# Optimization experiments

Hardware: AMD Instinct MI355X
Metric: run time of the kernel (lower is better)

The kernel has to match this reference:

```python
import jax, jax.numpy as jnp
import numpy as np


def _fps_indices(xyz, num_points):
    """Furthest point sampling. xyz: [B, N, 3] -> indices [B, num_points] (int32)."""
    B, N, _ = xyz.shape

    def step(carry, _):
        dist, farthest = carry                                   # dist: [B, N], farthest: [B]
        centroid = jnp.take_along_axis(xyz, farthest[:, None, None], axis=1)  # [B, 1, 3]
        d = jnp.sum((xyz - centroid) ** 2, axis=-1)              # [B, N]
        dist = jnp.minimum(dist, d)
        nxt = jnp.argmax(dist, axis=-1).astype(jnp.int32)        # [B]
        return (dist, nxt), farthest

    init = (jnp.full((B, N), jnp.inf, dtype=xyz.dtype),
            jnp.zeros((B,), dtype=jnp.int32))                    # convention: start at index 0
    _, idxs = jax.lax.scan(step, init, None, length=num_points)  # [num_points, B]
    return idxs.T                                                # [B, num_points]


def setup_inputs() -> dict:
    key = jax.random.key(0)
    B, C, N = 16, 3, 131072
    points = jax.random.normal(key, (B, C, N), dtype=jnp.float32)
    return {"points": points, "num_points": 2048}


def reference(points, num_points):
    # points: [B, 3, N] channels-first, as in the torch module
    xyz = jnp.transpose(points, (0, 2, 1))                       # [B, N, 3]
    idx = _fps_indices(xyz, num_points)                          # [B, num_points]
    # fps_gather_by_index: gather along the point dim of the channels-first tensor
    new_points = jnp.take_along_axis(points, idx[:, None, :], axis=2)  # [B, 3, num_points]
    return new_points
```

## Files before the change

### kernel.cpp

```cpp
#include <hip/hip_runtime.h>
#include <stdint.h>


#define NBATCH    16
#define NPTS      131072
#define SUBBLOCKS 16
#define NTHREADS  1024
#define CHUNK     8192
#define HALF      4096

typedef unsigned long long u64;

__device__ __forceinline__ u64 umax64(u64 a, u64 b) { return a > b ? a : b; }

__global__ __launch_bounds__(NTHREADS, 4)
void fps_kernel(const float* __restrict__ points,
                float* __restrict__ out,
                u64* __restrict__ slots, int M)
{
  __shared__ u64 wkeys[NTHREADS / 64];
  __shared__ u64 winner_s;

  const int bid   = blockIdx.x;
  const int xcd   = bid & 7;
  const int ord   = bid >> 3;
  const int batch = xcd * 2 + (ord >> 4);
  const int sub   = ord & 15;
  const int tid   = threadIdx.x;
  const int wave  = tid >> 6;
  const int lane  = tid & 63;

  const float* __restrict__ px = points + (size_t)batch * 3 * NPTS;
  const float* __restrict__ py = px + NPTS;
  const float* __restrict__ pz = px + 2 * NPTS;
  float* outb = out + (size_t)batch * 3 * M;
  u64* bslots = slots + (size_t)batch * 2 * SUBBLOCKS;

  const int cbase = sub * CHUNK;
  const int g0 = cbase + (tid << 2);
  const int g1 = g0 + HALF;

  float4 A0 = *(const float4*)(px + g0);
  float4 B0 = *(const float4*)(py + g0);
  float4 C0 = *(const float4*)(pz + g0);
  float4 A1 = *(const float4*)(px + g1);
  float4 B1 = *(const float4*)(py + g1);
  float4 C1 = *(const float4*)(pz + g1);
  float x0=A0.x, x1=A0.y, x2=A0.z, x3=A0.w, x4=A1.x, x5=A1.y, x6=A1.z, x7=A1.w;
  float y0=B0.x, y1=B0.y, y2=B0.z, y3=B0.w, y4=B1.x, y5=B1.y, y6=B1.z, y7=B1.w;
  float z0=C0.x, z1=C0.y, z2=C0.z, z3=C0.w, z4=C1.x, z5=C1.y, z6=C1.z, z7=C1.w;
  asm volatile("" :
    "+v"(x0),"+v"(x1),"+v"(x2),"+v"(x3),"+v"(x4),"+v"(x5),"+v"(x6),"+v"(x7),
    "+v"(y0),"+v"(y1),"+v"(y2),"+v"(y3),"+v"(y4),"+v"(y5),"+v"(y6),"+v"(y7),
    "+v"(z0),"+v"(z1),"+v"(z2),"+v"(z3),"+v"(z4),"+v"(z5),"+v"(z6),"+v"(z7));

  float d0, d1, d2, d3, d4, d5, d6, d7;
  d0 = d1 = d2 = d3 = d4 = d5 = d6 = d7 = __builtin_inff();

  if (sub == 0 && tid == 0) {
    outb[0]     = px[0];
    outb[M]     = py[0];
    outb[2 * M] = pz[0];
  }

  int sel = 0;
  for (int t = 1; t < M; ++t) {
    float cx = px[sel], cy = py[sel], cz = pz[sel];

    float best = -1.0f;
    int bidx = 0;
#define STEP(XX, YY, ZZ, DREG, IDX) { \
    float dx = __fsub_rn((XX), cx); \
    float dy = __fsub_rn((YY), cy); \
    float dz = __fsub_rn((ZZ), cz); \
    float dd = __builtin_fmaf(dz, dz, __builtin_fmaf(dy, dy, __fmul_rn(dx, dx))); \
    DREG = DREG < dd ? DREG : dd; \
    if (DREG > best) { best = DREG; bidx = (IDX); } }
    STEP(x0, y0, z0, d0, g0 + 0)
    STEP(x1, y1, z1, d1, g0 + 1)
    STEP(x2, y2, z2, d2, g0 + 2)
    STEP(x3, y3, z3, d3, g0 + 3)
    STEP(x4, y4, z4, d4, g1 + 0)
    STEP(x5, y5, z5, d5, g1 + 1)
    STEP(x6, y6, z6, d6, g1 + 2)
    STEP(x7, y7, z7, d7, g1 + 3)

    u64 key = ((u64)__float_as_uint(best) << 17) | (u64)((NPTS - 1) - bidx);

#pragma unroll
    for (int m = 32; m >= 1; m >>= 1) {
      u64 o = __shfl_xor(key, m, 64);
      key = umax64(key, o);
    }
    if (lane == 0) wkeys[wave] = key;
    __syncthreads();

    if (wave == 0) {
      u64 k = wkeys[lane & 15];
#pragma unroll
      for (int m = 8; m >= 1; m >>= 1) {
        u64 o = __shfl_xor(k, m, 64);
        k = umax64(k, o);
      }
      u64* par = bslots + (size_t)(t & 1) * SUBBLOCKS;
      if (lane == 0) {
        __hip_atomic_store(par + sub, ((u64)t << 49) | k,
                           __ATOMIC_RELAXED, __HIP_MEMORY_SCOPE_AGENT);
      }
      const u64* pp = par + (lane & 15);
      u64 v;
      for (;;) {
        v = __hip_atomic_load(pp, __ATOMIC_RELAXED, __HIP_MEMORY_SCOPE_AGENT);
        if (__ballot((unsigned)(v >> 49) == (unsigned)t) == ~0ull) break;
      }
#pragma unroll
      for (int m = 8; m >= 1; m >>= 1) {
        u64 o = __shfl_xor(v, m, 64);
        v = umax64(v, o);
      }
      if (lane == 0) winner_s = v;
    }
    __syncthreads();

    sel = (NPTS - 1) - (int)(winner_s & 0x1FFFF);

    if (sub == 0 && tid == 0) {
      outb[t]         = px[sel];
      outb[M + t]     = py[sel];
      outb[2 * M + t] = pz[sel];
    }
  }
}

extern "C" void kernel_launch(void* const* d_in, const int* in_sizes, int n_in,
                              void* d_out, int out_size, void* d_ws, size_t ws_size,
                              hipStream_t stream) {
  (void)in_sizes; (void)n_in; (void)ws_size;
  const float* points = (const float*)d_in[0];
  float* out = (float*)d_out;
  u64* slots = (u64*)d_ws;
  const int M = out_size / (NBATCH * 3);

  hipMemsetAsync(d_ws, 0, (size_t)NBATCH * 2 * SUBBLOCKS * sizeof(u64), stream);

  hipLaunchKernelGGL(fps_kernel, dim3(NBATCH * SUBBLOCKS), dim3(NTHREADS), 0,
                     stream, points, out, slots, M);
}
```

Measured before the change: 4.174 ms.

## Carry winner coordinates through cross-block slots and poll from all waves

Each block now publishes the winning point's x/y/z alongside its key in the global slot array, four u64 words per block. Every wave polls the slots and reduces them itself instead of wave 0 polling and then broadcasting through a second __syncthreads. This drops the per-iteration dependent global load of the centroid coordinates (px[sel]) and one block barrier from the critical serial path. The cost is wider slot writes, heavier polling traffic from 16 waves per block, and extra select logic to pick the winning coordinates from registers.

```diff
diff --git a/kernel.cpp b/kernel.cpp
--- a/kernel.cpp
+++ b/kernel.cpp
@@ -6,8 +6,10 @@
 #define NPTS      131072
 #define SUBBLOCKS 16
 #define NTHREADS  1024
+#define NWAVES    (NTHREADS / 64)
 #define CHUNK     8192
 #define HALF      4096
+#define SLOTW     4
 
 typedef unsigned long long u64;
 
@@ -18,8 +20,7 @@
                 float* __restrict__ out,
                 u64* __restrict__ slots, int M)
 {
-  __shared__ u64 wkeys[NTHREADS / 64];
-  __shared__ u64 winner_s;
+  __shared__ u64 W[NWAVES][SLOTW];
 
   const int bid   = blockIdx.x;
   const int xcd   = bid & 7;
@@ -29,12 +30,13 @@
   const int tid   = threadIdx.x;
   const int wave  = tid >> 6;
   const int lane  = tid & 63;
+  const int role  = lane & 3;
 
   const float* __restrict__ px = points + (size_t)batch * 3 * NPTS;
   const float* __restrict__ py = px + NPTS;
   const float* __restrict__ pz = px + 2 * NPTS;
   float* outb = out + (size_t)batch * 3 * M;
-  u64* bslots = slots + (size_t)batch * 2 * SUBBLOCKS;
+  u64* bslots = slots + (size_t)batch * 2 * SUBBLOCKS * SLOTW;
 
   const int cbase = sub * CHUNK;
   const int g0 = cbase + (tid << 2);
@@ -57,77 +59,97 @@
   float d0, d1, d2, d3, d4, d5, d6, d7;
   d0 = d1 = d2 = d3 = d4 = d5 = d6 = d7 = __builtin_inff();
 
+  float cx = px[0], cy = py[0], cz = pz[0];
   if (sub == 0 && tid == 0) {
-    outb[0]     = px[0];
-    outb[M]     = py[0];
-    outb[2 * M] = pz[0];
+    outb[0]     = cx;
+    outb[M]     = cy;
+    outb[2 * M] = cz;
   }
 
-  int sel = 0;
   for (int t = 1; t < M; ++t) {
-    float cx = px[sel], cy = py[sel], cz = pz[sel];
-
     float best = -1.0f;
-    int bidx = 0;
-#define STEP(XX, YY, ZZ, DREG, IDX) { \
+    int bidx = 0, bj = 0;
+#define STEP(XX, YY, ZZ, DREG, IDX, J) { \
     float dx = __fsub_rn((XX), cx); \
     float dy = __fsub_rn((YY), cy); \
     float dz = __fsub_rn((ZZ), cz); \
     float dd = __builtin_fmaf(dz, dz, __builtin_fmaf(dy, dy, __fmul_rn(dx, dx))); \
     DREG = DREG < dd ? DREG : dd; \
-    if (DREG > best) { best = DREG; bidx = (IDX); } }
-    STEP(x0, y0, z0, d0, g0 + 0)
-    STEP(x1, y1, z1, d1, g0 + 1)
-    STEP(x2, y2, z2, d2, g0 + 2)
-    STEP(x3, y3, z3, d3, g0 + 3)
-    STEP(x4, y4, z4, d4, g1 + 0)
-    STEP(x5, y5, z5, d5, g1 + 1)
-    STEP(x6, y6, z6, d6, g1 + 2)
-    STEP(x7, y7, z7, d7, g1 + 3)
+    if (DREG > best) { best = DREG; bidx = (IDX); bj = (J); } }
+    STEP(x0, y0, z0, d0, g0 + 0, 0)
+    STEP(x1, y1, z1, d1, g0 + 1, 1)
+    STEP(x2, y2, z2, d2, g0 + 2, 2)
+    STEP(x3, y3, z3, d3, g0 + 3, 3)
+    STEP(x4, y4, z4, d4, g1 + 0, 4)
+    STEP(x5, y5, z5, d5, g1 + 1, 5)
+    STEP(x6, y6, z6, d6, g1 + 2, 6)
+    STEP(x7, y7, z7, d7, g1 + 3, 7)
+
+    float bx = bj==0?x0:bj==1?x1:bj==2?x2:bj==3?x3:bj==4?x4:bj==5?x5:bj==6?x6:x7;
+    float by = bj==0?y0:bj==1?y1:bj==2?y2:bj==3?y3:bj==4?y4:bj==5?y5:bj==6?y6:y7;
+    float bz = bj==0?z0:bj==1?z1:bj==2?z2:bj==3?z3:bj==4?z4:bj==5?z5:bj==6?z6:z7;
 
     u64 key = ((u64)__float_as_uint(best) << 17) | (u64)((NPTS - 1) - bidx);
 
+    u64 wkey = key;
 #pragma unroll
-    for (int m = 32; m >= 1; m >>= 1) {
-      u64 o = __shfl_xor(key, m, 64);
-      key = umax64(key, o);
-    }
-    if (lane == 0) wkeys[wave] = key;
-    __syncthreads();
+    for (int m = 32; m >= 1; m >>= 1) wkey = umax64(wkey, __shfl_xor(wkey, m, 64));
 
-    if (wave == 0) {
-      u64 k = wkeys[lane & 15];
-#pragma unroll
-      for (int m = 8; m >= 1; m >>= 1) {
-        u64 o = __shfl_xor(k, m, 64);
-        k = umax64(k, o);
-      }
-      u64* par = bslots + (size_t)(t & 1) * SUBBLOCKS;
-      if (lane == 0) {
-        __hip_atomic_store(par + sub, ((u64)t << 49) | k,
-                           __ATOMIC_RELAXED, __HIP_MEMORY_SCOPE_AGENT);
-      }
-      const u64* pp = par + (lane & 15);
-      u64 v;
-      for (;;) {
-        v = __hip_atomic_load(pp, __ATOMIC_RELAXED, __HIP_MEMORY_SCOPE_AGENT);
-        if (__ballot((unsigned)(v >> 49) == (unsigned)t) == ~0ull) break;
-      }
-#pragma unroll
-      for (int m = 8; m >= 1; m >>= 1) {
-        u64 o = __shfl_xor(v, m, 64);
-        v = umax64(v, o);
-      }
-      if (lane == 0) winner_s = v;
+    if (wkey == key) {
+      W[wave][0] = key;
+      W[wave][1] = (u64)__float_as_uint(bx);
+      W[wave][2] = (u64)__float_as_uint(by);
+      W[wave][3] = (u64)__float_as_uint(bz);
     }
     __syncthreads();
 
-    sel = (NPTS - 1) - (int)(winner_s & 0x1FFFF);
+    u64* par = bslots + (size_t)(t & 1) * (SUBBLOCKS * SLOTW);
+
+    if (wave == 0) {
+      u64 mw = W[lane >> 2][role];
+      u64 mk = W[lane >> 2][0];
+#pragma unroll
+      for (int m = 32; m >= 4; m >>= 1) {
+        u64 ok = __shfl_xor(mk, m, 64);
+        u64 ow = __shfl_xor(mw, m, 64);
+        if (ok > mk) { mk = ok; mw = ow; }
+      }
+      if (lane < 4) {
+        u64 wd = (lane == 0) ? (((u64)t << 49) | mw)
+                             : ((mw & 0xFFFFFFFFull) | ((u64)t << 32));
+        __hip_atomic_store(par + (sub << 2) + lane, wd,
+                           __ATOMIC_RELAXED, __HIP_MEMORY_SCOPE_AGENT);
+      }
+    }
+
+    const u64* pp = par + lane;
+    u64 v;
+    for (;;) {
+      v = __hip_atomic_load(pp, __ATOMIC_RELAXED, __HIP_MEMORY_SCOPE_AGENT);
+      unsigned tag = (unsigned)(v >> (role ? 32 : 49));
+      if (__ballot(tag == (unsigned)t) == ~0ull) break;
+    }
+
+    {
+      u64 mk = __shfl(v, lane & 0x3C, 64) & 0x1FFFFFFFFFFFFull;
+      u64 mw = v;
+#pragma unroll
+      for (int m = 32; m >= 4; m >>= 1) {
+        u64 ok = __shfl_xor(mk, m, 64);
+        u64 ow = __shfl_xor(mw, m, 64);
+        if (ok > mk) { mk = ok; mw = ow; }
+      }
+      const int base = lane & 0x3C;
+      unsigned lo = (unsigned)mw;
+      cx = __uint_as_float((unsigned)__shfl((int)lo, base | 1, 64));
+      cy = __uint_as_float((unsigned)__shfl((int)lo, base | 2, 64));
+      cz = __uint_as_float((unsigned)__shfl((int)lo, base | 3, 64));
+    }
 
     if (sub == 0 && tid == 0) {
-      outb[t]         = px[sel];
-      outb[M + t]     = py[sel];
-      outb[2 * M + t] = pz[sel];
+      outb[t]         = cx;
+      outb[M + t]     = cy;
+      outb[2 * M + t] = cz;
     }
   }
 }
@@ -141,7 +163,8 @@
   u64* slots = (u64*)d_ws;
   const int M = out_size / (NBATCH * 3);
 
-  hipMemsetAsync(d_ws, 0, (size_t)NBATCH * 2 * SUBBLOCKS * sizeof(u64), stream);
+  hipMemsetAsync(d_ws, 0,
+                 (size_t)NBATCH * 2 * SUBBLOCKS * SLOTW * sizeof(u64), stream);
 
   hipLaunchKernelGGL(fps_kernel, dim3(NBATCH * SUBBLOCKS), dim3(NTHREADS), 0,
                      stream, points, out, slots, M);
```

New measurement: 6.961 ms. 1.67x slower.

## Interleave two batches per block to overlap cross-block sync with compute

Applied to the files above, without the earlier changes.

Each block now processes two batches (A and B) in an interleaved pipeline. While one batch's per-step global reduction is being polled across blocks, the block computes distances for the other batch. Winner coordinates are now published through the slots alongside the key, so the per-step dependent global load of the selected point is no longer needed. This hides inter-block barrier latency, at the cost of halving the block count (128 blocks), doubling the register usage per thread and adding more atomic traffic per step.

```diff
diff --git a/kernel.cpp b/kernel.cpp
--- a/kernel.cpp
+++ b/kernel.cpp
@@ -6,128 +6,183 @@
 #define NPTS      131072
 #define SUBBLOCKS 16
 #define NTHREADS  1024
+#define NWAVES    (NTHREADS / 64)
 #define CHUNK     8192
 #define HALF      4096
+#define SLOTW     4
+#define NBLOCKS   (8 * SUBBLOCKS)
 
 typedef unsigned long long u64;
 
 __device__ __forceinline__ u64 umax64(u64 a, u64 b) { return a > b ? a : b; }
+
+#define STEPX(XX, YY, ZZ, DREG, IDX, J, CX, CY, CZ) { \
+    float dx = __fsub_rn((XX), (CX)); \
+    float dy = __fsub_rn((YY), (CY)); \
+    float dz = __fsub_rn((ZZ), (CZ)); \
+    float dd = __builtin_fmaf(dz, dz, __builtin_fmaf(dy, dy, __fmul_rn(dx, dx))); \
+    DREG = DREG < dd ? DREG : dd; \
+    if (DREG > best) { best = DREG; bidx = (IDX); bj = (J); } }
+
+#define CDEP(P, Warr, CX, CY, CZ) { \
+    float best = -1.0f; int bidx = 0, bj = 0; \
+    STEPX(x##P##0, y##P##0, z##P##0, d##P##0, g0 + 0, 0, CX, CY, CZ) \
+    STEPX(x##P##1, y##P##1, z##P##1, d##P##1, g0 + 1, 1, CX, CY, CZ) \
+    STEPX(x##P##2, y##P##2, z##P##2, d##P##2, g0 + 2, 2, CX, CY, CZ) \
+    STEPX(x##P##3, y##P##3, z##P##3, d##P##3, g0 + 3, 3, CX, CY, CZ) \
+    STEPX(x##P##4, y##P##4, z##P##4, d##P##4, g1 + 0, 4, CX, CY, CZ) \
+    STEPX(x##P##5, y##P##5, z##P##5, d##P##5, g1 + 1, 5, CX, CY, CZ) \
+    STEPX(x##P##6, y##P##6, z##P##6, d##P##6, g1 + 2, 6, CX, CY, CZ) \
+    STEPX(x##P##7, y##P##7, z##P##7, d##P##7, g1 + 3, 7, CX, CY, CZ) \
+    float bx = bj==0?x##P##0:bj==1?x##P##1:bj==2?x##P##2:bj==3?x##P##3: \
+               bj==4?x##P##4:bj==5?x##P##5:bj==6?x##P##6:x##P##7; \
+    float by = bj==0?y##P##0:bj==1?y##P##1:bj==2?y##P##2:bj==3?y##P##3: \
+               bj==4?y##P##4:bj==5?y##P##5:bj==6?y##P##6:y##P##7; \
+    float bz = bj==0?z##P##0:bj==1?z##P##1:bj==2?z##P##2:bj==3?z##P##3: \
+               bj==4?z##P##4:bj==5?z##P##5:bj==6?z##P##6:z##P##7; \
+    u64 key = ((u64)__float_as_uint(best) << 17) | (u64)((NPTS - 1) - bidx); \
+    u64 wkey = key; \
+    _Pragma("unroll") \
+    for (int m = 32; m >= 1; m >>= 1) wkey = umax64(wkey, __shfl_xor(wkey, m, 64)); \
+    if (wkey == key) { \
+      Warr[wave][0] = key; \
+      Warr[wave][1] = (u64)__float_as_uint(bx); \
+      Warr[wave][2] = (u64)__float_as_uint(by); \
+      Warr[wave][3] = (u64)__float_as_uint(bz); \
+    } }
+
+#define RED_PUB(Warr, PAR, TAG) { \
+    u64 mw = Warr[lane >> 2][role]; \
+    u64 mk = Warr[lane >> 2][0]; \
+    _Pragma("unroll") \
+    for (int m = 32; m >= 4; m >>= 1) { \
+      u64 ok = __shfl_xor(mk, m, 64); \
+      u64 ow = __shfl_xor(mw, m, 64); \
+      if (ok > mk) { mk = ok; mw = ow; } } \
+    if (lane < 4) { \
+      u64 wd = (lane == 0) ? (((u64)(TAG) << 49) | mw) \
+                           : ((mw & 0xFFFFFFFFull) | ((u64)(TAG) << 32)); \
+      __hip_atomic_store((PAR) + (sub << 2) + lane, wd, \
+                         __ATOMIC_RELAXED, __HIP_MEMORY_SCOPE_AGENT); } }
+
+#define POLL_FIN(PAR, TAG, WIN) { \
+    const u64* pp = (PAR) + lane; \
+    u64 v; \
+    for (;;) { \
+      v = __hip_atomic_load(pp, __ATOMIC_RELAXED, __HIP_MEMORY_SCOPE_AGENT); \
+      unsigned tg = (unsigned)(v >> (role ? 32 : 49)); \
+      if (__ballot(tg == (unsigned)(TAG)) == ~0ull) break; } \
+    u64 mk = __shfl(v, lane & 0x3C, 64) & 0x1FFFFFFFFFFFFull; \
+    u64 mw = v; \
+    _Pragma("unroll") \
+    for (int m = 32; m >= 4; m >>= 1) { \
+      u64 ok = __shfl_xor(mk, m, 64); \
+      u64 ow = __shfl_xor(mw, m, 64); \
+      if (ok > mk) { mk = ok; mw = ow; } } \
+    if (lane >= 1 && lane <= 3) WIN[lane - 1] = __uint_as_float((unsigned)mw); }
 
 __global__ __launch_bounds__(NTHREADS, 4)
 void fps_kernel(const float* __restrict__ points,
                 float* __restrict__ out,
                 u64* __restrict__ slots, int M)
 {
-  __shared__ u64 wkeys[NTHREADS / 64];
-  __shared__ u64 winner_s;
-
-  const int bid   = blockIdx.x;
-  const int xcd   = bid & 7;
-  const int ord   = bid >> 3;
-  const int batch = xcd * 2 + (ord >> 4);
-  const int sub   = ord & 15;
-  const int tid   = threadIdx.x;
-  const int wave  = tid >> 6;
-  const int lane  = tid & 63;
-
-  const float* __restrict__ px = points + (size_t)batch * 3 * NPTS;
-  const float* __restrict__ py = px + NPTS;
-  const float* __restrict__ pz = px + 2 * NPTS;
-  float* outb = out + (size_t)batch * 3 * M;
-  u64* bslots = slots + (size_t)batch * 2 * SUBBLOCKS;
+  __shared__ u64 WA[NWAVES][SLOTW];
+  __shared__ u64 WB[NWAVES][SLOTW];
+  __shared__ float winA[4];
+  __shared__ float winB[4];
+
+  const int bid  = blockIdx.x;
+  const int xcd  = bid & 7;
+  const int sub  = bid >> 3;
+  const int tid  = threadIdx.x;
+  const int wave = tid >> 6;
+  const int lane = tid & 63;
+  const int role = lane & 3;
+
+  const int bA = xcd * 2;
+  const int bB = xcd * 2 + 1;
+
+  const float* __restrict__ pxA = points + (size_t)bA * 3 * NPTS;
+  const float* __restrict__ pyA = pxA + NPTS;
+  const float* __restrict__ pzA = pxA + 2 * NPTS;
+  const float* __restrict__ pxB = points + (size_t)bB * 3 * NPTS;
+  const float* __restrict__ pyB = pxB + NPTS;
+  const float* __restrict__ pzB = pxB + 2 * NPTS;
+  float* outA = out + (size_t)bA * 3 * M;
+  float* outB = out + (size_t)bB * 3 * M;
+  u64* slotsA = slots + (size_t)bA * 2 * SUBBLOCKS * SLOTW;
+  u64* slotsB = slots + (size_t)bB * 2 * SUBBLOCKS * SLOTW;
 
   const int cbase = sub * CHUNK;
   const int g0 = cbase + (tid << 2);
   const int g1 = g0 + HALF;
 
-  float4 A0 = *(const float4*)(px + g0);
-  float4 B0 = *(const float4*)(py + g0);
-  float4 C0 = *(const float4*)(pz + g0);
-  float4 A1 = *(const float4*)(px + g1);
-  float4 B1 = *(const float4*)(py + g1);
-  float4 C1 = *(const float4*)(pz + g1);
-  float x0=A0.x, x1=A0.y, x2=A0.z, x3=A0.w, x4=A1.x, x5=A1.y, x6=A1.z, x7=A1.w;
-  float y0=B0.x, y1=B0.y, y2=B0.z, y3=B0.w, y4=B1.x, y5=B1.y, y6=B1.z, y7=B1.w;
-  float z0=C0.x, z1=C0.y, z2=C0.z, z3=C0.w, z4=C1.x, z5=C1.y, z6=C1.z, z7=C1.w;
+  float4 t0, t1;
+  t0 = *(const float4*)(pxA + g0); t1 = *(const float4*)(pxA + g1);
+  float xA0=t0.x, xA1=t0.y, xA2=t0.z, xA3=t0.w, xA4=t1.x, xA5=t1.y, xA6=t1.z, xA7=t1.w;
+  t0 = *(const float4*)(pyA + g0); t1 = *(const float4*)(pyA + g1);
+  float yA0=t0.x, yA1=t0.y, yA2=t0.z, yA3=t0.w, yA4=t1.x, yA5=t1.y, yA6=t1.z, yA7=t1.w;
+  t0 = *(const float4*)(pzA + g0); t1 = *(const float4*)(pzA + g1);
+  float zA0=t0.x, zA1=t0.y, zA2=t0.z, zA3=t0.w, zA4=t1.x, zA5=t1.y, zA6=t1.z, zA7=t1.w;
+  t0 = *(const float4*)(pxB + g0); t1 = *(const float4*)(pxB + g1);
+  float xB0=t0.x, xB1=t0.y, xB2=t0.z, xB3=t0.w, xB4=t1.x, xB5=t1.y, xB6=t1.z, xB7=t1.w;
+  t0 = *(const float4*)(pyB + g0); t1 = *(const float4*)(pyB + g1);
+  float yB0=t0.x, yB1=t0.y, yB2=t0.z, yB3=t0.w, yB4=t1.x, yB5=t1.y, yB6=t1.z, yB7=t1.w;
+  t0 = *(const float4*)(pzB + g0); t1 = *(const float4*)(pzB + g1);
+  float zB0=t0.x, zB1=t0.y, zB2=t0.z, zB3=t0.w, zB4=t1.x, zB5=t1.y, zB6=t1.z, zB7=t1.w;
+
   asm volatile("" :
-    "+v"(x0),"+v"(x1),"+v"(x2),"+v"(x3),"+v"(x4),"+v"(x5),"+v"(x6),"+v"(x7),
-    "+v"(y0),"+v"(y1),"+v"(y2),"+v"(y3),"+v"(y4),"+v"(y5),"+v"(y6),"+v"(y7),
-    "+v"(z0),"+v"(z1),"+v"(z2),"+v"(z3),"+v"(z4),"+v"(z5),"+v"(z6),"+v"(z7));
-
-  float d0, d1, d2, d3, d4, d5, d6, d7;
-  d0 = d1 = d2 = d3 = d4 = d5 = d6 = d7 = __builtin_inff();
-
+    "+v"(xA0),"+v"(xA1),"+v"(xA2),"+v"(xA3),"+v"(xA4),"+v"(xA5),"+v"(xA6),"+v"(xA7),
+    "+v"(yA0),"+v"(yA1),"+v"(yA2),"+v"(yA3),"+v"(yA4),"+v"(yA5),"+v"(yA6),"+v"(yA7),
+    "+v"(zA0),"+v"(zA1),"+v"(zA2),"+v"(zA3),"+v"(zA4),"+v"(zA5),"+v"(zA6),"+v"(zA7));
+  asm volatile("" :
+    "+v"(xB0),"+v"(xB1),"+v"(xB2),"+v"(xB3),"+v"(xB4),"+v"(xB5),"+v"(xB6),"+v"(xB7),
+    "+v"(yB0),"+v"(yB1),"+v"(yB2),"+v"(yB3),"+v"(yB4),"+v"(yB5),"+v"(yB6),"+v"(yB7),
+    "+v"(zB0),"+v"(zB1),"+v"(zB2),"+v"(zB3),"+v"(zB4),"+v"(zB5),"+v"(zB6),"+v"(zB7));
+
+  float dA0, dA1, dA2, dA3, dA4, dA5, dA6, dA7;
+  float dB0, dB1, dB2, dB3, dB4, dB5, dB6, dB7;
+  dA0=dA1=dA2=dA3=dA4=dA5=dA6=dA7 = __builtin_inff();
+  dB0=dB1=dB2=dB3=dB4=dB5=dB6=dB7 = __builtin_inff();
+
+  float cAx = pxA[0], cAy = pyA[0], cAz = pzA[0];
+  float cBx = pxB[0], cBy = pyB[0], cBz = pzB[0];
   if (sub == 0 && tid == 0) {
-    outb[0]     = px[0];
-    outb[M]     = py[0];
-    outb[2 * M] = pz[0];
+    outA[0] = cAx; outA[M] = cAy; outA[2 * M] = cAz;
+    outB[0] = cBx; outB[M] = cBy; outB[2 * M] = cBz;
   }
 
-  int sel = 0;
+  if (M > 1) { CDEP(A, WA, cAx, cAy, cAz) }
+  __syncthreads();
+  if (M > 1 && wave == 0) { RED_PUB(WA, slotsA + 1 * (SUBBLOCKS * SLOTW), 1) }
+
   for (int t = 1; t < M; ++t) {
-    float cx = px[sel], cy = py[sel], cz = pz[sel];
-
-    float best = -1.0f;
-    int bidx = 0;
-#define STEP(XX, YY, ZZ, DREG, IDX) { \
-    float dx = __fsub_rn((XX), cx); \
-    float dy = __fsub_rn((YY), cy); \
-    float dz = __fsub_rn((ZZ), cz); \
-    float dd = __builtin_fmaf(dz, dz, __builtin_fmaf(dy, dy, __fmul_rn(dx, dx))); \
-    DREG = DREG < dd ? DREG : dd; \
-    if (DREG > best) { best = DREG; bidx = (IDX); } }
-    STEP(x0, y0, z0, d0, g0 + 0)
-    STEP(x1, y1, z1, d1, g0 + 1)
-    STEP(x2, y2, z2, d2, g0 + 2)
-    STEP(x3, y3, z3, d3, g0 + 3)
-    STEP(x4, y4, z4, d4, g1 + 0)
-    STEP(x5, y5, z5, d5, g1 + 1)
-    STEP(x6, y6, z6, d6, g1 + 2)
-    STEP(x7, y7, z7, d7, g1 + 3)
-
-    u64 key = ((u64)__float_as_uint(best) << 17) | (u64)((NPTS - 1) - bidx);
-
-#pragma unroll
-    for (int m = 32; m >= 1; m >>= 1) {
-      u64 o = __shfl_xor(key, m, 64);
-      key = umax64(key, o);
-    }
-    if (lane == 0) wkeys[wave] = key;
-    __syncthreads();
-
+    u64* parA  = slotsA + (size_t)(t & 1)       * (SUBBLOCKS * SLOTW);
+    u64* parA2 = slotsA + (size_t)((t + 1) & 1) * (SUBBLOCKS * SLOTW);
+    u64* parB  = slotsB + (size_t)(t & 1)       * (SUBBLOCKS * SLOTW);
+
+    CDEP(B, WB, cBx, cBy, cBz)
+    __syncthreads();
     if (wave == 0) {
-      u64 k = wkeys[lane & 15];
-#pragma unroll
-      for (int m = 8; m >= 1; m >>= 1) {
-        u64 o = __shfl_xor(k, m, 64);
-        k = umax64(k, o);
-      }
-      u64* par = bslots + (size_t)(t & 1) * SUBBLOCKS;
-      if (lane == 0) {
-        __hip_atomic_store(par + sub, ((u64)t << 49) | k,
-                           __ATOMIC_RELAXED, __HIP_MEMORY_SCOPE_AGENT);
-      }
-      const u64* pp = par + (lane & 15);
-      u64 v;
-      for (;;) {
-        v = __hip_atomic_load(pp, __ATOMIC_RELAXED, __HIP_MEMORY_SCOPE_AGENT);
-        if (__ballot((unsigned)(v >> 49) == (unsigned)t) == ~0ull) break;
-      }
-#pragma unroll
-      for (int m = 8; m >= 1; m >>= 1) {
-        u64 o = __shfl_xor(v, m, 64);
-        v = umax64(v, o);
-      }
-      if (lane == 0) winner_s = v;
-    }
-    __syncthreads();
-
-    sel = (NPTS - 1) - (int)(winner_s & 0x1FFFF);
-
+      RED_PUB(WB, parB, t)
+      POLL_FIN(parA, t, winA)
+    }
+    __syncthreads();
+    cAx = winA[0]; cAy = winA[1]; cAz = winA[2];
     if (sub == 0 && tid == 0) {
-      outb[t]         = px[sel];
-      outb[M + t]     = py[sel];
-      outb[2 * M + t] = pz[sel];
+      outA[t] = cAx; outA[M + t] = cAy; outA[2 * M + t] = cAz;
+    }
+
+    if (t < M - 1) { CDEP(A, WA, cAx, cAy, cAz) }
+    __syncthreads();
+    if (wave == 0) {
+      if (t < M - 1) { RED_PUB(WA, parA2, t + 1) }
+      POLL_FIN(parB, t, winB)
+    }
+    __syncthreads();
+    cBx = winB[0]; cBy = winB[1]; cBz = winB[2];
+    if (sub == 0 && tid == 0) {
+      outB[t] = cBx; outB[M + t] = cBy; outB[2 * M + t] = cBz;
     }
   }
 }
@@ -141,8 +196,9 @@
   u64* slots = (u64*)d_ws;
   const int M = out_size / (NBATCH * 3);
 
-  hipMemsetAsync(d_ws, 0, (size_t)NBATCH * 2 * SUBBLOCKS * sizeof(u64), stream);
-
-  hipLaunchKernelGGL(fps_kernel, dim3(NBATCH * SUBBLOCKS), dim3(NTHREADS), 0,
+  hipMemsetAsync(d_ws, 0,
+                 (size_t)NBATCH * 2 * SUBBLOCKS * SLOTW * sizeof(u64), stream);
+
+  hipLaunchKernelGGL(fps_kernel, dim3(NBLOCKS), dim3(NTHREADS), 0,
                      stream, points, out, slots, M);
 }
```

New measurement: 9.106 ms. +118.2%, slower.

## Double-buffer cross-block spin loads and prefetch winner coordinates in wave 0

Applied to the files above, without the earlier changes.

The cross-block barrier poll now keeps two outstanding system-coherent loads in flight through inline assembly, so each check overlaps the next request instead of serialising load latency. After the winner is found, each of the 16 polling lanes speculatively loads the coordinates of its own candidate before the reduction. The lane whose key equals the maximum writes them to shared memory, so all threads read the centroid from LDS instead of issuing dependent global loads at the start of the next step. This shortens the critical path of every sampling iteration at the cost of extra loads per poll and hand-written waitcnt management, which could be fragile.

```diff
diff --git a/kernel.cpp b/kernel.cpp
--- a/kernel.cpp
+++ b/kernel.cpp
@@ -19,7 +19,7 @@
                 u64* __restrict__ slots, int M)
 {
   __shared__ u64 wkeys[NTHREADS / 64];
-  __shared__ u64 winner_s;
+  __shared__ float winC[3];
 
   const int bid   = blockIdx.x;
   const int xcd   = bid & 7;
@@ -62,11 +62,9 @@
     outb[M]     = py[0];
     outb[2 * M] = pz[0];
   }
+  float cx = px[0], cy = py[0], cz = pz[0];
 
-  int sel = 0;
   for (int t = 1; t < M; ++t) {
-    float cx = px[sel], cy = py[sel], cz = pz[sel];
-
     float best = -1.0f;
     int bidx = 0;
 #define STEP(XX, YY, ZZ, DREG, IDX) { \
@@ -108,26 +106,46 @@
                            __ATOMIC_RELAXED, __HIP_MEMORY_SCOPE_AGENT);
       }
       const u64* pp = par + (lane & 15);
-      u64 v;
+
+      asm volatile("s_waitcnt vmcnt(0)" ::: "memory");
+
+      u64 va, vb, v;
+      asm volatile("global_load_dwordx2 %0, %1, off sc0 sc1"
+                   : "=v"(va) : "v"(pp) : "memory");
+      asm volatile("global_load_dwordx2 %0, %1, off sc0 sc1"
+                   : "=v"(vb) : "v"(pp) : "memory");
       for (;;) {
-        v = __hip_atomic_load(pp, __ATOMIC_RELAXED, __HIP_MEMORY_SCOPE_AGENT);
-        if (__ballot((unsigned)(v >> 49) == (unsigned)t) == ~0ull) break;
+        asm volatile("s_waitcnt vmcnt(1)" ::: "memory");
+        __builtin_amdgcn_sched_barrier(0);
+        if (__ballot((unsigned)(va >> 49) == (unsigned)t) == ~0ull) { v = va; break; }
+        asm volatile("global_load_dwordx2 %0, %1, off sc0 sc1"
+                     : "=v"(va) : "v"(pp) : "memory");
+        asm volatile("s_waitcnt vmcnt(1)" ::: "memory");
+        __builtin_amdgcn_sched_barrier(0);
+        if (__ballot((unsigned)(vb >> 49) == (unsigned)t) == ~0ull) { v = vb; break; }
+        asm volatile("global_load_dwordx2 %0, %1, off sc0 sc1"
+                     : "=v"(vb) : "v"(pp) : "memory");
       }
+
+      int cidx = (NPTS - 1) - (int)(v & 0x1FFFF);
+      float qx = 0.f, qy = 0.f, qz = 0.f;
+      if (lane < 16) { qx = px[cidx]; qy = py[cidx]; qz = pz[cidx]; }
+      u64 kk = v;
 #pragma unroll
       for (int m = 8; m >= 1; m >>= 1) {
-        u64 o = __shfl_xor(v, m, 64);
-        v = umax64(v, o);
+        u64 o = __shfl_xor(kk, m, 64);
+        kk = umax64(kk, o);
       }
-      if (lane == 0) winner_s = v;
+      if (lane < 16 && v == kk) { winC[0] = qx; winC[1] = qy; winC[2] = qz; }
+      asm volatile("s_waitcnt vmcnt(0)" :: "v"(va), "v"(vb) : "memory");
     }
     __syncthreads();
 
-    sel = (NPTS - 1) - (int)(winner_s & 0x1FFFF);
-
+    cx = winC[0]; cy = winC[1]; cz = winC[2];
     if (sub == 0 && tid == 0) {
-      outb[t]         = px[sel];
-      outb[M + t]     = py[sel];
-      outb[2 * M + t] = pz[sel];
+      outb[t]         = cx;
+      outb[M + t]     = cy;
+      outb[2 * M + t] = cz;
     }
   }
 }
```

After: 4.206 ms. No clear change (+0.8%).
